# Performance work log

Hardware: AMD Instinct MI355X
Metric: run time of the kernel (lower is better)

Reference implementation:

```python
import jax, jax.numpy as jnp
import numpy as np

B, N, D = 1, 2048, 1024
L, H, DH = 4, 16, 64
INNER = H * DH            # 1024, == D
FF = int(D * 4.0)         # 4096 (GEGLU inner)
SCALE = DH ** -0.5
LN_EPS = 1e-5


def setup_inputs() -> dict:
    key = jax.random.key(0)
    ks = jax.random.split(key, 8)
    w = 0.02
    inp = {
        'x': jax.random.normal(ks[0], (B, N, D), jnp.float32),
        'mask': jnp.ones((B, N), dtype=bool),
        # stacked per-layer params (leading dim L)
        'Wqkv': jax.random.normal(ks[1], (L, D, 3 * INNER), jnp.float32) * w,
        'Wo': jax.random.normal(ks[2], (L, INNER, D), jnp.float32) * w,
        'bo': jnp.zeros((L, D), jnp.float32),
        'ln1_g': jnp.ones((L, D), jnp.float32),
        'ln1_b': jnp.zeros((L, D), jnp.float32),
        'ln2_g': jnp.ones((L, D), jnp.float32),
        'ln2_b': jnp.zeros((L, D), jnp.float32),
        'ls1': jnp.full((L, D), 0.1, jnp.float32),  # LayerScale init_eps=0.1 (depth<=18)
        'ls2': jnp.full((L, D), 0.1, jnp.float32),
        'W1': jax.random.normal(ks[3], (L, D, 2 * FF), jnp.float32) * w,
        'b1': jnp.zeros((L, 2 * FF), jnp.float32),
        'W2': jax.random.normal(ks[4], (L, FF, D), jnp.float32) * w,
        'b2': jnp.zeros((L, D), jnp.float32),
    }
    return inp


def _layernorm(x, g, b):
    mu = jnp.mean(x, axis=-1, keepdims=True)
    var = jnp.mean(jnp.square(x - mu), axis=-1, keepdims=True)
    return (x - mu) * jax.lax.rsqrt(var + LN_EPS) * g + b


def _forward(x, mask, Wqkv, Wo, bo, ln1_g, ln1_b, ln2_g, ln2_b, ls1, ls2, W1, b1, W2, b2):
    n = x.shape[1]
    causal = jnp.arange(n)[None, :] > jnp.arange(n)[:, None]  # True = masked
    valid = mask[:, None, None, :] & ~causal[None, None]       # (B,1,N,N) True = keep
    for l in range(L):
        # --- attention sublayer: x + LayerScale(PreNorm(Attn))(x) ---
        h = _layernorm(x, ln1_g[l], ln1_b[l])
        qkv = h @ Wqkv[l]                                      # (B,N,3*INNER)
        q, k, v = jnp.split(qkv, 3, axis=-1)
        q = q.reshape(B, n, H, DH).transpose(0, 2, 1, 3) * SCALE
        k = k.reshape(B, n, H, DH).transpose(0, 2, 1, 3)
        v = v.reshape(B, n, H, DH).transpose(0, 2, 1, 3)
        dots = jnp.einsum('bhid,bhjd->bhij', q, k)             # (B,H,N,N)
        neg = -jnp.finfo(dots.dtype).max
        dots = jnp.where(valid, dots, neg)
        attn = jax.nn.softmax(dots, axis=-1)                   # stable_softmax, temp=1
        o = jnp.einsum('bhij,bhjd->bhid', attn, v)
        o = o.transpose(0, 2, 1, 3).reshape(B, n, INNER)
        o = o @ Wo[l] + bo[l]
        x = x + o * ls1[l]
        # --- feedforward sublayer: x + LayerScale(PreNorm(GEGLU-FFN))(x) ---
        h = _layernorm(x, ln2_g[l], ln2_b[l])
        u = h @ W1[l] + b1[l]                                  # (B,N,2*FF)
        a, g = jnp.split(u, 2, axis=-1)
        f = (a * jax.nn.gelu(g, approximate=False)) @ W2[l] + b2[l]
        x = x + f * ls2[l]
    return x


def reference(x, mask, Wqkv, Wo, bo, ln1_g, ln1_b, ln2_g, ln2_b, ls1, ls2, W1, b1, W2, b2):
    return _forward(x, mask, Wqkv, Wo, bo, ln1_g, ln1_b, ln2_g, ln2_b, ls1, ls2, W1, b1, W2, b2)
```

## Files before the change

### kernel.cpp

```cpp
#include <hip/hip_runtime.h>
#include <hip/hip_bf16.h>
#include <math.h>

#define LN_EPS 1e-5f
#define ATT_SCALE 0.125f

typedef __bf16 bf16x8 __attribute__((ext_vector_type(8)));
typedef float f32x4 __attribute__((ext_vector_type(4)));

__device__ __forceinline__ unsigned short f2bf(float f){
  unsigned int u = __builtin_bit_cast(unsigned int, f);
  u += 0x7fffu + ((u >> 16) & 1u);
  return (unsigned short)(u >> 16);
}
__device__ __forceinline__ float bfbits2f(unsigned int lo16){
  return __builtin_bit_cast(float, lo16 << 16);
}

__global__ __launch_bounds__(256) void ln_kernel(
    const float* __restrict__ X, const float* __restrict__ g,
    const float* __restrict__ b, unsigned short* __restrict__ H)
{
  __shared__ float red[4];
  int row = blockIdx.x, t = threadIdx.x;
  const float4 xv = ((const float4*)(X + (size_t)row*1024))[t];
  float s = xv.x + xv.y + xv.z + xv.w;
  #pragma unroll
  for (int o=32;o;o>>=1) s += __shfl_down(s,o);
  if ((t&63)==0) red[t>>6] = s;
  __syncthreads();
  float mu = (red[0]+red[1]+red[2]+red[3]) * (1.f/1024.f);
  __syncthreads();
  float dx = xv.x-mu, dy = xv.y-mu, dz = xv.z-mu, dw = xv.w-mu;
  float s2 = dx*dx+dy*dy+dz*dz+dw*dw;
  #pragma unroll
  for (int o=32;o;o>>=1) s2 += __shfl_down(s2,o);
  if ((t&63)==0) red[t>>6] = s2;
  __syncthreads();
  float var = (red[0]+red[1]+red[2]+red[3]) * (1.f/1024.f);
  float rs = rsqrtf(var + LN_EPS);
  const float4 gv = ((const float4*)g)[t];
  const float4 bv = ((const float4*)b)[t];
  ushort4 o4;
  o4.x = f2bf(dx*rs*gv.x + bv.x);
  o4.y = f2bf(dy*rs*gv.y + bv.y);
  o4.z = f2bf(dz*rs*gv.z + bv.z);
  o4.w = f2bf(dw*rs*gv.w + bv.w);
  ((ushort4*)(H + (size_t)row*1024))[t] = o4;
}

template<int SK, int DO_LN>
__global__ __launch_bounds__(256) void redln_kernel(
    const unsigned short* __restrict__ P, float* __restrict__ X,
    const float* __restrict__ bias, const float* __restrict__ scale,
    const float* __restrict__ g, const float* __restrict__ b,
    unsigned short* __restrict__ H)
{
  __shared__ float red[4];
  int row = blockIdx.x, t = threadIdx.x;
  size_t off = (size_t)row*1024 + t*4;
  float4 xv = *(const float4*)(X + off);
  float4 pv;
  {
    uint2 u = *(const uint2*)(P + off);
    pv.x = bfbits2f(u.x & 0xffffu); pv.y = bfbits2f(u.x >> 16);
    pv.z = bfbits2f(u.y & 0xffffu); pv.w = bfbits2f(u.y >> 16);
  }
  #pragma unroll
  for (int c=1;c<SK;c++){
    uint2 u = *(const uint2*)(P + (size_t)c*2048*1024 + off);
    pv.x += bfbits2f(u.x & 0xffffu); pv.y += bfbits2f(u.x >> 16);
    pv.z += bfbits2f(u.y & 0xffffu); pv.w += bfbits2f(u.y >> 16);
  }
  const float4 bv = ((const float4*)bias)[t];
  const float4 sv = ((const float4*)scale)[t];
  xv.x += (pv.x+bv.x)*sv.x;
  xv.y += (pv.y+bv.y)*sv.y;
  xv.z += (pv.z+bv.z)*sv.z;
  xv.w += (pv.w+bv.w)*sv.w;
  *(float4*)(X + off) = xv;
  if (DO_LN){
    float s = xv.x + xv.y + xv.z + xv.w;
    #pragma unroll
    for (int o=32;o;o>>=1) s += __shfl_down(s,o);
    if ((t&63)==0) red[t>>6] = s;
    __syncthreads();
    float mu = (red[0]+red[1]+red[2]+red[3]) * (1.f/1024.f);
    __syncthreads();
    float dx = xv.x-mu, dy = xv.y-mu, dz = xv.z-mu, dw = xv.w-mu;
    float s2 = dx*dx+dy*dy+dz*dz+dw*dw;
    #pragma unroll
    for (int o=32;o;o>>=1) s2 += __shfl_down(s2,o);
    if ((t&63)==0) red[t>>6] = s2;
    __syncthreads();
    float var = (red[0]+red[1]+red[2]+red[3]) * (1.f/1024.f);
    float rs = rsqrtf(var + LN_EPS);
    const float4 gv = ((const float4*)g)[t];
    const float4 lbv = ((const float4*)b)[t];
    ushort4 o4;
    o4.x = f2bf(dx*rs*gv.x + lbv.x);
    o4.y = f2bf(dy*rs*gv.y + lbv.y);
    o4.z = f2bf(dz*rs*gv.z + lbv.z);
    o4.w = f2bf(dw*rs*gv.w + lbv.w);
    ((ushort4*)(H + (size_t)row*1024))[t] = o4;
  }
}

__global__ __launch_bounds__(256) void trc_kernel(
    const float* __restrict__ W, unsigned short* __restrict__ WT, int K, int N)
{
  __shared__ float tile[64][65];
  const float* Wz = W + (size_t)blockIdx.z*K*N;
  unsigned short* WTz = WT + (size_t)blockIdx.z*K*N;
  int n0 = blockIdx.x*64, k0 = blockIdx.y*64;
  int t = threadIdx.x;
  int tx = t & 63, ty = t >> 6;
  #pragma unroll
  for (int p=0;p<16;p++){
    int r = ty*16+p;
    tile[r][tx] = Wz[(size_t)(k0+r)*N + n0 + tx];
  }
  __syncthreads();
  int kc = t & 31, tb = t >> 5;
  #pragma unroll
  for (int p=0;p<8;p++){
    int nr = tb + p*8;
    unsigned int lo = f2bf(tile[2*kc][nr]);
    unsigned int hi = f2bf(tile[2*kc+1][nr]);
    ((unsigned int*)(WTz + (size_t)(n0+nr)*K + k0))[kc] = lo | (hi<<16);
  }
}

__global__ __launch_bounds__(256) void trc_w1_kernel(
    const float* __restrict__ W, unsigned short* __restrict__ WT)
{
  __shared__ float tile[64][65];
  const float* Wz = W + (size_t)blockIdx.z*1024*8192;
  unsigned short* WTz = WT + (size_t)blockIdx.z*1024*8192;
  int n0 = blockIdx.x*64, k0 = blockIdx.y*64;
  int ca = (n0>>5)*16;
  int t = threadIdx.x;
  int tx = t & 63, ty = t >> 6;
  #pragma unroll
  for (int p=0;p<16;p++){
    int r = ty*16+p;
    int col = (tx < 32) ? (ca + tx) : (ca + 4064 + tx);
    tile[r][tx] = Wz[(size_t)(k0+r)*8192 + col];
  }
  __syncthreads();
  int kc = t & 31, tb = t >> 5;
  #pragma unroll
  for (int p=0;p<8;p++){
    int nr = tb + p*8;
    int rr = nr & 31;
    int vcol = (nr>>5)*16 + (rr&15) + ((rr>>4)<<5);
    unsigned int lo = f2bf(tile[2*kc][vcol]);
    unsigned int hi = f2bf(tile[2*kc+1][vcol]);
    ((unsigned int*)(WTz + (size_t)(n0+nr)*1024 + k0))[kc] = lo | (hi<<16);
  }
}

template<int MODE, int SWZ>
__global__ __launch_bounds__(256) void gemm_bt(
    const unsigned short* __restrict__ A, const unsigned short* __restrict__ BT,
    int M, int N, int K,
    unsigned short* __restrict__ Obf,
    const float* __restrict__ bias)
{
  __shared__ unsigned short Asm[2][128*64];
  __shared__ unsigned short Bsm[2][128*64];
  int t = threadIdx.x;
  int lane = t & 63;
  int w = t >> 6, wm = w >> 1, wn = w & 1;

  int bn, bm;
  if (SWZ){
    int nwg = gridDim.x * gridDim.y;
    int wg = blockIdx.y * gridDim.x + blockIdx.x;
    int cpx = nwg >> 3;
    int swz = (wg & 7) * cpx + (wg >> 3);
    bn = swz % gridDim.x; bm = swz / gridDim.x;
  } else {
    bn = blockIdx.x; bm = blockIdx.y;
  }

  f32x4 acc[4][4] = {};
  int ktBeg = 0, ktEnd = K >> 6;
  if (MODE == 3){
    int per = (K >> 6) / gridDim.z;
    ktBeg = blockIdx.z * per;
    ktEnd = ktBeg + per;
  }

  int srow = t >> 3, ssc = t & 7;
  auto STAGE = [&](int kt, int buf){
    #pragma unroll
    for (int c=0;c<4;c++){
      int row = c*32 + srow;
      int gc = ssc ^ (row & 7);
      const unsigned short* sa = A  + (size_t)(bm*128 + row)*K + kt*64 + gc*8;
      const unsigned short* sb = BT + (size_t)(bn*128 + row)*K + kt*64 + gc*8;
      __builtin_amdgcn_global_load_lds(
        (const __attribute__((address_space(1))) unsigned int*)sa,
        (__attribute__((address_space(3))) unsigned int*)(&Asm[buf][(c*256 + (t & ~63))*8]),
        16, 0, 0);
      __builtin_amdgcn_global_load_lds(
        (const __attribute__((address_space(1))) unsigned int*)sb,
        (__attribute__((address_space(3))) unsigned int*)(&Bsm[buf][(c*256 + (t & ~63))*8]),
        16, 0, 0);
    }
  };

  STAGE(ktBeg, 0);
  __syncthreads();
  int cur = 0;
  for (int kt = ktBeg; kt < ktEnd; ++kt){
    if (kt + 1 < ktEnd) STAGE(kt + 1, cur ^ 1);
    #pragma unroll
    for (int kk=0;kk<2;kk++){
      bf16x8 aF[4], bF[4];
      #pragma unroll
      for (int m=0;m<4;m++){
        int row = wm*64 + m*16 + (lane&15);
        int ch = kk*4 + (lane>>4);
        aF[m] = *(const bf16x8*)&Asm[cur][row*64 + (ch ^ (row&7))*8];
      }
      #pragma unroll
      for (int n=0;n<4;n++){
        int row = wn*64 + n*16 + (lane&15);
        int ch = kk*4 + (lane>>4);
        bF[n] = *(const bf16x8*)&Bsm[cur][row*64 + (ch ^ (row&7))*8];
      }
      __builtin_amdgcn_s_setprio(1);
      #pragma unroll
      for (int m=0;m<4;m++)
        #pragma unroll
        for (int n=0;n<4;n++)
          acc[m][n] = __builtin_amdgcn_mfma_f32_16x16x32_bf16(aF[m], bF[n], acc[m][n], 0,0,0);
      __builtin_amdgcn_s_setprio(0);
    }
    __syncthreads();
    cur ^= 1;
  }

  unsigned short* ep = &Asm[0][0];
  int colg = lane & 15;
  int r0 = wm*64 + (lane>>4)*4;
  if (MODE==4){
    float b1a[2], b1g[2];
    #pragma unroll
    for (int p=0;p<2;p++){
      int oc = (bn*4 + wn*2 + p)*16 + colg;
      b1a[p] = bias[oc];
      b1g[p] = bias[oc + 4096];
    }
    #pragma unroll
    for (int m=0;m<4;m++){
      #pragma unroll
      for (int p=0;p<2;p++){
        int cw = (wn*2 + p)*16 + colg;
        #pragma unroll
        for (int j=0;j<4;j++){
          float va = acc[m][2*p][j]   + b1a[p];
          float vg = acc[m][2*p+1][j] + b1g[p];
          float f = va * (0.5f * vg * (1.f + erff(vg * 0.70710678118f)));
          ep[(r0 + m*16 + j)*64 + cw] = f2bf(f);
        }
      }
    }
    __syncthreads();
    #pragma unroll
    for (int i=0;i<4;i++){
      int idx = i*256 + t;
      int row = idx >> 3, ch = idx & 7;
      *(uint4*)&Obf[(size_t)(bm*128+row)*4096 + bn*64 + ch*8] = *(const uint4*)&ep[row*64 + ch*8];
    }
    return;
  }
  #pragma unroll
  for (int m=0;m<4;m++)
    #pragma unroll
    for (int n=0;n<4;n++){
      int cw = wn*64 + n*16 + colg;
      #pragma unroll
      for (int j=0;j<4;j++)
        ep[(r0 + m*16 + j)*128 + cw] = f2bf(acc[m][n][j]);
    }
  __syncthreads();
  size_t zoff = (MODE==3) ? (size_t)blockIdx.z*((size_t)M*N) : 0;
  #pragma unroll
  for (int i=0;i<8;i++){
    int idx = i*256 + t;
    int row = idx >> 4, ch = idx & 15;
    *(uint4*)&Obf[zoff + (size_t)(bm*128+row)*N + bn*128 + ch*8] = *(const uint4*)&ep[row*128 + ch*8];
  }
}

__global__ __launch_bounds__(256) void vtr_kernel(
    const unsigned short* __restrict__ qkv, unsigned short* __restrict__ VT)
{
  __shared__ unsigned int tile[64][33];
  int h = blockIdx.y;
  int n0 = blockIdx.x * 64;
  int t = threadIdx.x;
  #pragma unroll
  for (int p=0;p<8;p++){
    int idx = p*256 + t;
    int r = idx >> 5, c = idx & 31;
    tile[r][c] = *(const unsigned int*)(qkv + (size_t)(n0+r)*3072 + 2048 + h*64 + c*2);
  }
  __syncthreads();
  #pragma unroll
  for (int p=0;p<8;p++){
    int idx = p*256 + t;
    int d = idx >> 5, c = idx & 31;
    unsigned int a = tile[2*c][d>>1];
    unsigned int b = tile[2*c+1][d>>1];
    unsigned int lo = (d&1) ? (a>>16) : (a & 0xffffu);
    unsigned int hi = (d&1) ? (b>>16) : (b & 0xffffu);
    *(unsigned int*)(VT + (size_t)h*131072 + (size_t)d*2048 + n0 + c*2) = lo | (hi<<16);
  }
}

__global__ __launch_bounds__(256) void flash_attn(
    const unsigned short* __restrict__ qkv,
    const unsigned short* __restrict__ VT,
    unsigned short* __restrict__ O)
{
  __shared__ unsigned short Klds[2][64*64];
  __shared__ unsigned short Vlds[2][64*64];
  __shared__ unsigned short Plds[4][16*72];
  __shared__ float fbuf[4][16];
  __shared__ float lbuf[4][16];

  int t = threadIdx.x;
  int lane = t & 63;
  int w = t >> 6;
  int q15 = lane & 15, l16 = lane >> 4;

  int bid = blockIdx.x;
  int x = bid & 7, r = bid >> 3;
  int h = 2*x + (r & 1);
  int q = r >> 1;
  int qt = (q < 16) ? q : 47 - q;
  int q0 = qt * 64;

  bf16x8 qF[2];
  int qrow = q0 + w*16 + q15;
  #pragma unroll
  for (int db=0; db<2; db++)
    qF[db] = *(const bf16x8*)(qkv + (size_t)qrow*3072 + h*64 + db*32 + l16*8);

  int srow = t >> 3, ssc = t & 7;
  auto STAGE = [&](int kt, int buf){
    int k0 = kt*64;
    #pragma unroll
    for (int c=0;c<2;c++){
      int row = c*32 + srow;
      int gc = ssc ^ (row & 7);
      const unsigned short* sk = qkv + (size_t)(k0+row)*3072 + 1024 + h*64 + gc*8;
      const unsigned short* sv = VT + (size_t)h*131072 + (size_t)row*2048 + k0 + gc*8;
      __builtin_amdgcn_global_load_lds(
        (const __attribute__((address_space(1))) unsigned int*)sk,
        (__attribute__((address_space(3))) unsigned int*)(&Klds[buf][(c*256 + (t & ~63))*8]),
        16, 0, 0);
      __builtin_amdgcn_global_load_lds(
        (const __attribute__((address_space(1))) unsigned int*)sv,
        (__attribute__((address_space(3))) unsigned int*)(&Vlds[buf][(c*256 + (t & ~63))*8]),
        16, 0, 0);
    }
  };

  f32x4 o[4] = {};
  float m_run = -1e30f, l_run = 0.f;

  STAGE(0, 0);
  __syncthreads();
  int cur = 0;
  for (int kt = 0; kt <= qt; ++kt){
    if (kt < qt) STAGE(kt + 1, cur ^ 1);

    f32x4 s[4] = {};
    #pragma unroll
    for (int km=0;km<4;km++){
      #pragma unroll
      for (int db=0;db<2;db++){
        int row = km*16 + q15;
        int ch = db*4 + l16;
        bf16x8 kF = *(const bf16x8*)&Klds[cur][row*64 + (ch ^ (row&7))*8];
        s[km] = __builtin_amdgcn_mfma_f32_16x16x32_bf16(kF, qF[db], s[km], 0,0,0);
      }
    }

    bool diag = (kt == qt);
    float pmax = -1e30f;
    #pragma unroll
    for (int km=0;km<4;km++){
      #pragma unroll
      for (int j=0;j<4;j++){
        float sv = s[km][j] * ATT_SCALE;
        if (diag){
          int kg = km*16 + l16*4 + j;
          int qg = w*16 + q15;
          if (kg > qg) sv = -1e30f;
        }
        s[km][j] = sv;
        pmax = fmaxf(pmax, sv);
      }
    }
    pmax = fmaxf(pmax, __shfl_xor(pmax, 16));
    pmax = fmaxf(pmax, __shfl_xor(pmax, 32));

    if (!__all(pmax - m_run <= 8.f)){
      float m_new = fmaxf(m_run, pmax);
      float f = __expf(m_run - m_new);
      m_run = m_new;
      l_run *= f;
      if (l16 == 0) fbuf[w][q15] = f;
      f32x4 fv = *(f32x4*)&fbuf[w][l16*4];
      #pragma unroll
      for (int n=0;n<4;n++) o[n] *= fv;
    }

    float lsum = 0.f;
    #pragma unroll
    for (int km=0;km<4;km++){
      float p0 = __expf(s[km][0]-m_run);
      float p1 = __expf(s[km][1]-m_run);
      float p2 = __expf(s[km][2]-m_run);
      float p3 = __expf(s[km][3]-m_run);
      lsum += (p0+p1)+(p2+p3);
      unsigned int v0 = (unsigned int)f2bf(p0) | ((unsigned int)f2bf(p1)<<16);
      unsigned int v1 = (unsigned int)f2bf(p2) | ((unsigned int)f2bf(p3)<<16);
      *(uint2*)&Plds[w][q15*72 + km*16 + l16*4] = make_uint2(v0,v1);
    }
    lsum += __shfl_xor(lsum,16);
    lsum += __shfl_xor(lsum,32);
    l_run += lsum;

    #pragma unroll
    for (int kb=0;kb<2;kb++){
      bf16x8 aP = *(const bf16x8*)&Plds[w][q15*72 + kb*32 + l16*8];
      #pragma unroll
      for (int n=0;n<4;n++){
        int row = n*16 + q15;
        int ch = kb*4 + l16;
        bf16x8 vF = *(const bf16x8*)&Vlds[cur][row*64 + (ch ^ (row&7))*8];
        o[n] = __builtin_amdgcn_mfma_f32_16x16x32_bf16(aP, vF, o[n], 0,0,0);
      }
    }
    __syncthreads();
    cur ^= 1;
  }

  if (l16 == 0) lbuf[w][q15] = 1.f / l_run;
  f32x4 lv = *(f32x4*)&lbuf[w][l16*4];

  #pragma unroll
  for (int n=0;n<4;n++){
    #pragma unroll
    for (int j=0;j<4;j++){
      int row = q0 + w*16 + l16*4 + j;
      int col = h*64 + n*16 + q15;
      O[(size_t)row*1024 + col] = f2bf(o[n][j]*lv[j]);
    }
  }
}

extern "C" void kernel_launch(void* const* d_in, const int* in_sizes, int n_in,
                              void* d_out, int out_size, void* d_ws, size_t ws_size,
                              hipStream_t stream)
{
  (void)in_sizes; (void)n_in; (void)out_size; (void)ws_size;
  const float* x_in = (const float*)d_in[0];
  const float* Wqkv = (const float*)d_in[2];
  const float* Wo   = (const float*)d_in[3];
  const float* bo   = (const float*)d_in[4];
  const float* ln1g = (const float*)d_in[5];
  const float* ln1b = (const float*)d_in[6];
  const float* ln2g = (const float*)d_in[7];
  const float* ln2b = (const float*)d_in[8];
  const float* ls1  = (const float*)d_in[9];
  const float* ls2  = (const float*)d_in[10];
  const float* W1   = (const float*)d_in[11];
  const float* b1   = (const float*)d_in[12];
  const float* W2   = (const float*)d_in[13];
  const float* b2   = (const float*)d_in[14];
  float* X = (float*)d_out;

  char* ws = (char*)d_ws;
  unsigned short* WTq = (unsigned short*)(ws);
  unsigned short* WTo = (unsigned short*)(ws + (24u<<20));
  unsigned short* WT1 = (unsigned short*)(ws + (32u<<20));
  unsigned short* WT2 = (unsigned short*)(ws + (96u<<20));
  unsigned short* hb  = (unsigned short*)(ws + (128u<<20));
  unsigned short* qu  = (unsigned short*)(ws + (132u<<20));
  unsigned short* VTg = (unsigned short*)(ws + (144u<<20));
  unsigned short* of  = (unsigned short*)(ws + (148u<<20));
  unsigned short* PTb = (unsigned short*)(ws + (164u<<20));

  hipMemcpyAsync(d_out, (const void*)x_in, (size_t)2048*1024*4,
                 hipMemcpyDeviceToDevice, stream);

  trc_kernel<<<dim3(3072/64,1024/64,4),256,0,stream>>>(Wqkv, WTq, 1024, 3072);
  trc_kernel<<<dim3(1024/64,1024/64,4),256,0,stream>>>(Wo,   WTo, 1024, 1024);
  trc_w1_kernel<<<dim3(8192/64,1024/64,4),256,0,stream>>>(W1, WT1);
  trc_kernel<<<dim3(1024/64,4096/64,4),256,0,stream>>>(W2,   WT2, 4096, 1024);

  for (int l = 0; l < 4; ++l){
    if (l == 0)
      ln_kernel<<<2048,256,0,stream>>>(X, ln1g, ln1b, hb);
    gemm_bt<0,0><<<dim3(3072/128,2048/128),256,0,stream>>>(hb, WTq + (size_t)l*3072*1024,
        2048,3072,1024, qu, nullptr);
    vtr_kernel<<<dim3(32,16),256,0,stream>>>(qu, VTg);
    flash_attn<<<512,256,0,stream>>>(qu, VTg, of);
    gemm_bt<3,1><<<dim3(1024/128,2048/128,2),256,0,stream>>>(of, WTo + (size_t)l*1024*1024,
        2048,1024,1024, PTb, nullptr);
    redln_kernel<2,1><<<2048,256,0,stream>>>(PTb, X, bo + l*1024, ls1 + l*1024,
        ln2g + l*1024, ln2b + l*1024, hb);
    gemm_bt<4,0><<<dim3(8192/128,2048/128),256,0,stream>>>(hb, WT1 + (size_t)l*8192*1024,
        2048,8192,1024, of, b1 + (size_t)l*8192);
    gemm_bt<3,1><<<dim3(1024/128,2048/128,4),256,0,stream>>>(of, WT2 + (size_t)l*1024*4096,
        2048,1024,4096, PTb, nullptr);
    if (l < 3)
      redln_kernel<4,1><<<2048,256,0,stream>>>(PTb, X, b2 + l*1024, ls2 + l*1024,
          ln1g + (l+1)*1024, ln1b + (l+1)*1024, hb);
    else
      redln_kernel<4,0><<<2048,256,0,stream>>>(PTb, X, b2 + l*1024, ls2 + l*1024,
          nullptr, nullptr, nullptr);
  }
}
```

Before: 790.7 us.

## Replace W1 GEMM with 256x256-tile 8-wave kernel using direct global-to-LDS loads

Adds a dedicated GEGLU W1 GEMM kernel with 256x256 output tiles, 512 threads (8 waves), global_load_lds async copies into double-buffered swizzled LDS, and a fine-grained interleaved schedule of half-tile loads and MFMA quarters. The goal is more data reuse per tile and better overlap of memory loads with MFMA compute on the largest GEMM. The GEGLU epilogue now writes straight to global with scattered 2-byte stores instead of staging through LDS, and the old MODE 4 epilogue is removed. The new kernel uses the full 128KB of LDS per block and many barriers, which could limit occupancy or add synchronisation overhead.

```diff
diff --git a/kernel.cpp b/kernel.cpp
--- a/kernel.cpp
+++ b/kernel.cpp
@@ -246,37 +246,6 @@
   unsigned short* ep = &Asm[0][0];
   int colg = lane & 15;
   int r0 = wm*64 + (lane>>4)*4;
-  if (MODE==4){
-    float b1a[2], b1g[2];
-    #pragma unroll
-    for (int p=0;p<2;p++){
-      int oc = (bn*4 + wn*2 + p)*16 + colg;
-      b1a[p] = bias[oc];
-      b1g[p] = bias[oc + 4096];
-    }
-    #pragma unroll
-    for (int m=0;m<4;m++){
-      #pragma unroll
-      for (int p=0;p<2;p++){
-        int cw = (wn*2 + p)*16 + colg;
-        #pragma unroll
-        for (int j=0;j<4;j++){
-          float va = acc[m][2*p][j]   + b1a[p];
-          float vg = acc[m][2*p+1][j] + b1g[p];
-          float f = va * (0.5f * vg * (1.f + erff(vg * 0.70710678118f)));
-          ep[(r0 + m*16 + j)*64 + cw] = f2bf(f);
-        }
-      }
-    }
-    __syncthreads();
-    #pragma unroll
-    for (int i=0;i<4;i++){
-      int idx = i*256 + t;
-      int row = idx >> 3, ch = idx & 7;
-      *(uint4*)&Obf[(size_t)(bm*128+row)*4096 + bn*64 + ch*8] = *(const uint4*)&ep[row*64 + ch*8];
-    }
-    return;
-  }
   #pragma unroll
   for (int m=0;m<4;m++)
     #pragma unroll
@@ -293,6 +262,134 @@
     int idx = i*256 + t;
     int row = idx >> 4, ch = idx & 15;
     *(uint4*)&Obf[zoff + (size_t)(bm*128+row)*N + bn*128 + ch*8] = *(const uint4*)&ep[row*128 + ch*8];
+  }
+}
+
+#define G8F() asm volatile("" ::: "memory")
+#define G8BAR() do { G8F(); __builtin_amdgcn_s_barrier(); G8F(); } while(0)
+#define G8VW4() asm volatile("s_waitcnt vmcnt(4)" ::: "memory")
+#define G8VW0() asm volatile("s_waitcnt vmcnt(0)" ::: "memory")
+
+__global__ __launch_bounds__(512,2) void gemm8_w1(
+    const unsigned short* __restrict__ A, const unsigned short* __restrict__ BT,
+    unsigned short* __restrict__ Fout, const float* __restrict__ b1)
+{
+  __shared__ __attribute__((aligned(16))) unsigned short lds[65536];
+  const int K = 1024, nkt = 16;
+  int t = threadIdx.x;
+  int lane = t & 63;
+  int w = t >> 6;
+  int wm = w >> 2, wn = w & 3;
+  int bh = wn >> 1;
+  int q15 = lane & 15, l16 = lane >> 4;
+  int bn = blockIdx.x, bm = blockIdx.y;
+  int rA0 = bm*256, rB0 = bn*256;
+
+  auto STG = [&](const unsigned short* Mat, int r0, int kt, int half, int buf, int isB){
+    int base = buf*32768 + isB*16384 + half*8192;
+    #pragma unroll
+    for (int l=0;l<2;l++){
+      int li = l*512 + t;
+      int row = li >> 3, sc = li & 7;
+      int gc = sc ^ (row & 7);
+      const unsigned short* src = Mat + (size_t)(r0 + half*128 + row)*K + kt*64 + gc*8;
+      __builtin_amdgcn_global_load_lds(
+        (const __attribute__((address_space(1))) unsigned int*)src,
+        (__attribute__((address_space(3))) unsigned int*)(&lds[base + (l*512 + (t & ~63))*8]),
+        16, 0, 0);
+    }
+  };
+
+  f32x4 acc[8][4] = {};
+  bf16x8 aF[4][2], bF0[2][2], bF1[2][2];
+
+  auto RD_A = [&](int mh, int buf){
+    int base = buf*32768 + wm*8192;
+    #pragma unroll
+    for (int m=0;m<4;m++){
+      int r = mh*64 + m*16 + q15;
+      #pragma unroll
+      for (int kk=0;kk<2;kk++)
+        aF[m][kk] = *(const bf16x8*)&lds[base + r*64 + (((kk*4+l16) ^ (r&7))*8)];
+    }
+  };
+  auto RD_B = [&](bf16x8 (*dst)[2], int h, int buf){
+    int base = buf*32768 + 16384 + bh*8192;
+    #pragma unroll
+    for (int n=0;n<2;n++){
+      int r = (wn&1)*64 + (h*2+n)*16 + q15;
+      #pragma unroll
+      for (int kk=0;kk<2;kk++)
+        dst[n][kk] = *(const bf16x8*)&lds[base + r*64 + (((kk*4+l16) ^ (r&7))*8)];
+    }
+  };
+  auto MF = [&](int mb, int nb, bf16x8 (*bf)[2]){
+    __builtin_amdgcn_s_setprio(1);
+    #pragma unroll
+    for (int m=0;m<4;m++)
+      #pragma unroll
+      for (int n=0;n<2;n++)
+        #pragma unroll
+        for (int kk=0;kk<2;kk++)
+          acc[mb+m][nb+n] = __builtin_amdgcn_mfma_f32_16x16x32_bf16(
+              aF[m][kk], bf[n][kk], acc[mb+m][nb+n], 0,0,0);
+    __builtin_amdgcn_s_setprio(0);
+  };
+
+  STG(A,  rA0, 0, 0, 0, 0);
+  STG(A,  rA0, 0, 1, 0, 0);
+  STG(BT, rB0, 0, 0, 0, 1);
+  STG(BT, rB0, 0, 1, 0, 1);
+  STG(BT, rB0, 1, 0, 1, 1);
+  STG(A,  rA0, 1, 0, 1, 0);
+  G8VW4();
+  G8BAR();
+
+  for (int kt = 0; kt < nkt; ++kt){
+    int buf = kt & 1, nb = buf ^ 1;
+    if (kt + 1 < nkt) STG(A, rA0, kt+1, 1, nb, 0);
+    RD_A(0, buf); RD_B(bF0, 0, buf);
+    G8BAR();
+    MF(0, 0, bF0);
+    G8BAR();
+    if (kt + 1 < nkt) STG(BT, rB0, kt+1, 1, nb, 1);
+    RD_B(bF1, 1, buf);
+    G8BAR();
+    MF(0, 2, bF1);
+    G8BAR();
+    if (kt + 2 < nkt) STG(BT, rB0, kt+2, 0, buf, 1);
+    RD_A(1, buf);
+    G8BAR();
+    MF(4, 0, bF0);
+    G8BAR();
+    if (kt + 2 < nkt) STG(A, rA0, kt+2, 0, buf, 0);
+    G8BAR();
+    MF(4, 2, bF1);
+    if (kt == nkt-2) { G8VW0(); } else if (kt+1 < nkt) { G8VW4(); }
+    G8BAR();
+  }
+
+  float b1a[2], b1g[2];
+  #pragma unroll
+  for (int p=0;p<2;p++){
+    int oc = (bn*8 + wn*2 + p)*16 + q15;
+    b1a[p] = b1[oc];
+    b1g[p] = b1[oc + 4096];
+  }
+  #pragma unroll
+  for (int m=0;m<8;m++){
+    int gr0 = bm*256 + wm*128 + m*16 + l16*4;
+    #pragma unroll
+    for (int p=0;p<2;p++){
+      int ocol = (bn*8 + wn*2 + p)*16 + q15;
+      #pragma unroll
+      for (int j=0;j<4;j++){
+        float va = acc[m][2*p][j]   + b1a[p];
+        float vg = acc[m][2*p+1][j] + b1g[p];
+        float f = va * (0.5f * vg * (1.f + erff(vg * 0.70710678118f)));
+        Fout[(size_t)(gr0+j)*4096 + ocol] = f2bf(f);
+      }
+    }
   }
 }
 
@@ -518,8 +615,8 @@
         2048,1024,1024, PTb, nullptr);
     redln_kernel<2,1><<<2048,256,0,stream>>>(PTb, X, bo + l*1024, ls1 + l*1024,
         ln2g + l*1024, ln2b + l*1024, hb);
-    gemm_bt<4,0><<<dim3(8192/128,2048/128),256,0,stream>>>(hb, WT1 + (size_t)l*8192*1024,
-        2048,8192,1024, of, b1 + (size_t)l*8192);
+    gemm8_w1<<<dim3(8192/256,2048/256),512,0,stream>>>(hb, WT1 + (size_t)l*8192*1024,
+        of, b1 + (size_t)l*8192);
     gemm_bt<3,1><<<dim3(1024/128,2048/128,4),256,0,stream>>>(of, WT2 + (size_t)l*1024*4096,
         2048,1024,4096, PTb, nullptr);
     if (l < 3)
```

Measured after the change: 742.8 us, median of 2. -6.1%, faster.

## Split W1 GEMM over K and move GEGLU into a separate reduce kernel

Applied to the files above, without the earlier changes.

The FFN up-projection GEMM no longer applies bias and GEGLU in its epilogue. It now runs as a two-way split-K GEMM that writes bf16 partial products. A new row-wise kernel sums the two partials, adds the bias, applies the erf-based GELU gating and writes the bf16 activation. This doubles the block count and shortens each block's K loop to improve GPU occupancy. In exchange it adds a full extra write and read of a 2x2048x8192 partial buffer, one more launch, and extra bf16 rounding of the partials.

```diff
diff --git a/kernel.cpp b/kernel.cpp
--- a/kernel.cpp
+++ b/kernel.cpp
@@ -106,6 +106,37 @@
   }
 }
 
+__global__ __launch_bounds__(256) void redgeglu_kernel(
+    const unsigned short* __restrict__ P, const float* __restrict__ b1,
+    unsigned short* __restrict__ F)
+{
+  int row = blockIdx.x, t = threadIdx.x;
+  const unsigned short* p0 = P + (size_t)row*8192 + t*32;
+  const unsigned short* p1 = p0 + (size_t)2048*8192;
+  unsigned int q0[16], q1[16];
+  #pragma unroll
+  for (int i=0;i<4;i++){
+    ((uint4*)q0)[i] = ((const uint4*)p0)[i];
+    ((uint4*)q1)[i] = ((const uint4*)p1)[i];
+  }
+  const float* b1a = b1 + t*16;
+  const float* b1g = b1 + 4096 + t*16;
+  unsigned int outw[8];
+  #pragma unroll
+  for (int i=0;i<8;i++){
+    float a0 = bfbits2f(q0[i]&0xffffu)   + bfbits2f(q1[i]&0xffffu)   + b1a[2*i];
+    float a1 = bfbits2f(q0[i]>>16)       + bfbits2f(q1[i]>>16)       + b1a[2*i+1];
+    float g0 = bfbits2f(q0[8+i]&0xffffu) + bfbits2f(q1[8+i]&0xffffu) + b1g[2*i];
+    float g1 = bfbits2f(q0[8+i]>>16)     + bfbits2f(q1[8+i]>>16)     + b1g[2*i+1];
+    float f0 = a0 * (0.5f*g0*(1.f+erff(g0*0.70710678118f)));
+    float f1 = a1 * (0.5f*g1*(1.f+erff(g1*0.70710678118f)));
+    outw[i] = (unsigned int)f2bf(f0) | ((unsigned int)f2bf(f1)<<16);
+  }
+  unsigned short* fo = F + (size_t)row*4096 + t*16;
+  ((uint4*)fo)[0] = *(uint4*)&outw[0];
+  ((uint4*)fo)[1] = *(uint4*)&outw[4];
+}
+
 __global__ __launch_bounds__(256) void trc_kernel(
     const float* __restrict__ W, unsigned short* __restrict__ WT, int K, int N)
 {
@@ -246,37 +277,6 @@
   unsigned short* ep = &Asm[0][0];
   int colg = lane & 15;
   int r0 = wm*64 + (lane>>4)*4;
-  if (MODE==4){
-    float b1a[2], b1g[2];
-    #pragma unroll
-    for (int p=0;p<2;p++){
-      int oc = (bn*4 + wn*2 + p)*16 + colg;
-      b1a[p] = bias[oc];
-      b1g[p] = bias[oc + 4096];
-    }
-    #pragma unroll
-    for (int m=0;m<4;m++){
-      #pragma unroll
-      for (int p=0;p<2;p++){
-        int cw = (wn*2 + p)*16 + colg;
-        #pragma unroll
-        for (int j=0;j<4;j++){
-          float va = acc[m][2*p][j]   + b1a[p];
-          float vg = acc[m][2*p+1][j] + b1g[p];
-          float f = va * (0.5f * vg * (1.f + erff(vg * 0.70710678118f)));
-          ep[(r0 + m*16 + j)*64 + cw] = f2bf(f);
-        }
-      }
-    }
-    __syncthreads();
-    #pragma unroll
-    for (int i=0;i<4;i++){
-      int idx = i*256 + t;
-      int row = idx >> 3, ch = idx & 7;
-      *(uint4*)&Obf[(size_t)(bm*128+row)*4096 + bn*64 + ch*8] = *(const uint4*)&ep[row*64 + ch*8];
-    }
-    return;
-  }
   #pragma unroll
   for (int m=0;m<4;m++)
     #pragma unroll
@@ -518,8 +518,9 @@
         2048,1024,1024, PTb, nullptr);
     redln_kernel<2,1><<<2048,256,0,stream>>>(PTb, X, bo + l*1024, ls1 + l*1024,
         ln2g + l*1024, ln2b + l*1024, hb);
-    gemm_bt<4,0><<<dim3(8192/128,2048/128),256,0,stream>>>(hb, WT1 + (size_t)l*8192*1024,
-        2048,8192,1024, of, b1 + (size_t)l*8192);
+    gemm_bt<3,0><<<dim3(8192/128,2048/128,2),256,0,stream>>>(hb, WT1 + (size_t)l*8192*1024,
+        2048,8192,1024, PTb, nullptr);
+    redgeglu_kernel<<<2048,256,0,stream>>>(PTb, b1 + (size_t)l*8192, of);
     gemm_bt<3,1><<<dim3(1024/128,2048/128,4),256,0,stream>>>(of, WT2 + (size_t)l*1024*4096,
         2048,1024,4096, PTb, nullptr);
     if (l < 3)
```

New measurement: 862.9 us. 9.1% more time.
